# Performance work log

Measured on AMD Instinct MI355X. Metric: run time of the kernel, lower is better.

Reference implementation:

```python
import jax, jax.numpy as jnp
import numpy as np

ROI = 31            # roi_size (odd)
HALF = ROI // 2     # tf.cast(roi_size/2, int32) == 15


def setup_inputs() -> dict:
    key = jax.random.key(0)
    k1, k2, k3, k4 = jax.random.split(key, 4)
    B, H, W, C, N = 16, 256, 256, 32, 4096
    encoded_poses = jax.random.normal(k1, (B, H, W, C), dtype=jnp.float32)
    b = jax.random.randint(k2, (N, 1), 0, B)
    y = jax.random.randint(k3, (N, 1), 0, H)
    x = jax.random.randint(k4, (N, 1), 0, W)
    roi_centers = jnp.concatenate([b, y, x], axis=1).astype(jnp.int32)
    return {"encoded_poses": encoded_poses, "roi_centers": roi_centers}


def reference(encoded_poses, roi_centers):
    # encoded_poses: [B, H, W, C]; roi_centers: [N, 3] = (batch, y, x)
    H, W = encoded_poses.shape[1], encoded_poses.shape[2]
    off = jnp.arange(ROI, dtype=roi_centers.dtype) - HALF          # [ROI]
    b = roi_centers[:, 0]                                          # [N]
    rows = roi_centers[:, 1, None] + off                           # [N, ROI]
    cols = roi_centers[:, 2, None] + off                           # [N, ROI]
    # Out-of-bounds positions get zero padding (as in tf.pad of the original).
    rmask = (rows >= 0) & (rows < H)
    cmask = (cols >= 0) & (cols < W)
    rc = jnp.clip(rows, 0, H - 1)
    cc = jnp.clip(cols, 0, W - 1)
    # Batched gather: [N, ROI, ROI, C]
    cuts = encoded_poses[b[:, None, None], rc[:, :, None], cc[:, None, :], :]
    mask = (rmask[:, :, None] & cmask[:, None, :])[..., None]
    return jnp.where(mask, cuts, jnp.zeros((), dtype=cuts.dtype))
```

## Files before the change

kernel.cpp:

```cpp
#include <hip/hip_runtime.h>

#define ROI 31
#define HALF 15
#define H_DIM 256
#define W_DIM 256
#define C_DIM 32
#define NBKT 4096

typedef float vfloat4 __attribute__((ext_vector_type(4)));

__global__ __launch_bounds__(1024) void sort_kernel(
    const int* __restrict__ centers, int* __restrict__ perm,
    int* __restrict__ off, int N)
{
    __shared__ int hist[NBKT];
    __shared__ int base[NBKT];
    __shared__ int partial[1024];
    const int t = threadIdx.x;

    for (int k = t; k < NBKT; k += 1024) hist[k] = 0;
    __syncthreads();

    for (int i = t; i < N; i += 1024) {
        const int key = (centers[3 * i] << 8) | centers[3 * i + 1];
        atomicAdd(&hist[key], 1);
    }
    __syncthreads();

    const int s0 = hist[4 * t], s1 = hist[4 * t + 1];
    const int s2 = hist[4 * t + 2], s3 = hist[4 * t + 3];
    const int loc = s0 + s1 + s2 + s3;
    partial[t] = loc;
    __syncthreads();
    for (int o = 1; o < 1024; o <<= 1) {
        int v = (t >= o) ? partial[t - o] : 0;
        __syncthreads();
        partial[t] += v;
        __syncthreads();
    }
    const int ex = partial[t] - loc;
    base[4 * t]     = ex;
    base[4 * t + 1] = ex + s0;
    base[4 * t + 2] = ex + s0 + s1;
    base[4 * t + 3] = ex + s0 + s1 + s2;
    __syncthreads();

    for (int k = t; k < NBKT; k += 1024) off[k] = base[k];
    if (t == 0) off[NBKT] = N;
    for (int k = t; k < NBKT; k += 1024) hist[k] = 0;
    __syncthreads();

    for (int i = t; i < N; i += 1024) {
        const int key = (centers[3 * i] << 8) | centers[3 * i + 1];
        const int pos = base[key] + atomicAdd(&hist[key], 1);
        perm[pos] = i;
    }
}

__global__ __launch_bounds__(256) void strip_scatter_kernel(
    const float* __restrict__ poses, const int* __restrict__ centers,
    const int* __restrict__ perm, const int* __restrict__ off,
    float* __restrict__ out)
{
    __shared__ vfloat4 row_lds[W_DIM * C_DIM / 4];

    const int strip = blockIdx.x;
    const int b  = strip >> 8;
    const int rr = strip & (H_DIM - 1);
    const int t  = threadIdx.x;

    const vfloat4* src_row = reinterpret_cast<const vfloat4*>(
        poses + ((size_t)b * H_DIM + rr) * W_DIM * C_DIM);
    #pragma unroll
    for (int i = 0; i < 8; ++i)
        row_lds[i * 256 + t] = src_row[i * 256 + t];
    __syncthreads();

    const int ylo = max(rr - HALF, 0), yhi = min(rr + HALF, H_DIM - 1);
    const int start = off[(b << 8) | ylo];
    const int end   = off[((b << 8) | yhi) + 1];

    const int pc = t >> 3;
    const int q  = t & 7;
    if (pc >= ROI) return;

    for (int pos = start; pos < end; ++pos) {
        const int n = perm[pos];
        const int y = centers[3 * n + 1];
        const int x = centers[3 * n + 2];
        const int r  = rr - (y - HALF);
        const int cc = x - HALF + pc;
        const bool cok = (cc >= 0) && (cc < W_DIM);
        const int ccc = min(max(cc, 0), W_DIM - 1);
        vfloat4 v = cok ? row_lds[ccc * 8 + q] : (vfloat4)0.0f;
        float* dst = out + (((size_t)n * ROI + r) * ROI + pc) * C_DIM + q * 4;
        __builtin_nontemporal_store(v, reinterpret_cast<vfloat4*>(dst));
    }
}

__global__ __launch_bounds__(256) void zero_rows_kernel(
    const int* __restrict__ centers, float* __restrict__ out)
{
    const int n = blockIdx.x;
    const int y = centers[3 * n + 1];
    if (y >= HALF && y <= H_DIM - 1 + HALF - ROI + 1) {  }
    const int t = threadIdx.x;
    if (t >= ROI * (C_DIM / 4)) return;
    const int pc = t >> 3;
    const int q  = t & 7;
    const vfloat4 z = (vfloat4)0.0f;

    const int rlo_end   = max(HALF - y, 0);
    const int rhi_start = min(H_DIM - 1 + HALF - y + 1, ROI);
    for (int r = 0; r < rlo_end; ++r) {
        float* dst = out + (((size_t)n * ROI + r) * ROI + pc) * C_DIM + q * 4;
        __builtin_nontemporal_store(z, reinterpret_cast<vfloat4*>(dst));
    }
    for (int r = rhi_start; r < ROI; ++r) {
        float* dst = out + (((size_t)n * ROI + r) * ROI + pc) * C_DIM + q * 4;
        __builtin_nontemporal_store(z, reinterpret_cast<vfloat4*>(dst));
    }
}

extern "C" void kernel_launch(void* const* d_in, const int* in_sizes, int n_in,
                              void* d_out, int out_size, void* d_ws, size_t ws_size,
                              hipStream_t stream) {
    const float* poses   = (const float*)d_in[0];
    const int*   centers = (const int*)d_in[1];
    float*       out     = (float*)d_out;

    const int N = in_sizes[1] / 3;
    const int B = in_sizes[0] / (H_DIM * W_DIM * C_DIM);

    int* perm = (int*)d_ws;
    int* off  = perm + N;

    sort_kernel<<<dim3(1), dim3(1024), 0, stream>>>(centers, perm, off, N);
    strip_scatter_kernel<<<dim3(B * H_DIM), dim3(256), 0, stream>>>(poses, centers, perm, off, out);
    zero_rows_kernel<<<dim3(N), dim3(256), 0, stream>>>(centers, out);
}
```

Measured before the change: 116.4 us.

## Fuse border zero-fill into strip scatter and pack center coords into sort records

The strip grid gains virtual rows above and below the image, so the same scatter kernel writes zeros for out-of-range ROI rows. This removes the separate zero_rows kernel and its launch. The sort also emits packed (index, y, x) records, so the scatter loop no longer does a dependent gather from perm into centers. In exchange, 30 extra strip blocks per batch do store-only work, and the packing limits N to what fits above 16 bits.

```diff
diff --git a/kernel.cpp b/kernel.cpp
--- a/kernel.cpp
+++ b/kernel.cpp
@@ -6,11 +6,12 @@
 #define W_DIM 256
 #define C_DIM 32
 #define NBKT 4096
+#define VROWS (H_DIM + 2*HALF)
 
 typedef float vfloat4 __attribute__((ext_vector_type(4)));
 
 __global__ __launch_bounds__(1024) void sort_kernel(
-    const int* __restrict__ centers, int* __restrict__ perm,
+    const int* __restrict__ centers, int* __restrict__ sorted,
     int* __restrict__ off, int N)
 {
     __shared__ int hist[NBKT];
@@ -51,30 +52,33 @@
     __syncthreads();
 
     for (int i = t; i < N; i += 1024) {
-        const int key = (centers[3 * i] << 8) | centers[3 * i + 1];
+        const int b = centers[3 * i], y = centers[3 * i + 1], x = centers[3 * i + 2];
+        const int key = (b << 8) | y;
         const int pos = base[key] + atomicAdd(&hist[key], 1);
-        perm[pos] = i;
+        sorted[pos] = (i << 16) | (y << 8) | x;
     }
 }
 
 __global__ __launch_bounds__(256) void strip_scatter_kernel(
-    const float* __restrict__ poses, const int* __restrict__ centers,
-    const int* __restrict__ perm, const int* __restrict__ off,
-    float* __restrict__ out)
+    const float* __restrict__ poses, const int* __restrict__ sorted,
+    const int* __restrict__ off, float* __restrict__ out)
 {
     __shared__ vfloat4 row_lds[W_DIM * C_DIM / 4];
 
     const int strip = blockIdx.x;
-    const int b  = strip >> 8;
-    const int rr = strip & (H_DIM - 1);
+    const int b  = strip / VROWS;
+    const int rr = strip % VROWS - HALF;
     const int t  = threadIdx.x;
+    const bool real = ((unsigned)rr < (unsigned)H_DIM);
 
-    const vfloat4* src_row = reinterpret_cast<const vfloat4*>(
-        poses + ((size_t)b * H_DIM + rr) * W_DIM * C_DIM);
-    #pragma unroll
-    for (int i = 0; i < 8; ++i)
-        row_lds[i * 256 + t] = src_row[i * 256 + t];
-    __syncthreads();
+    if (real) {
+        const vfloat4* src_row = reinterpret_cast<const vfloat4*>(
+            poses + ((size_t)b * H_DIM + rr) * W_DIM * C_DIM);
+        #pragma unroll
+        for (int i = 0; i < 8; ++i)
+            row_lds[i * 256 + t] = src_row[i * 256 + t];
+        __syncthreads();
+    }
 
     const int ylo = max(rr - HALF, 0), yhi = min(rr + HALF, H_DIM - 1);
     const int start = off[(b << 8) | ylo];
@@ -85,40 +89,20 @@
     if (pc >= ROI) return;
 
     for (int pos = start; pos < end; ++pos) {
-        const int n = perm[pos];
-        const int y = centers[3 * n + 1];
-        const int x = centers[3 * n + 2];
+        const int rec = sorted[pos];
+        const int n = rec >> 16;
+        const int y = (rec >> 8) & 255;
+        const int x = rec & 255;
         const int r  = rr - (y - HALF);
         const int cc = x - HALF + pc;
-        const bool cok = (cc >= 0) && (cc < W_DIM);
-        const int ccc = min(max(cc, 0), W_DIM - 1);
-        vfloat4 v = cok ? row_lds[ccc * 8 + q] : (vfloat4)0.0f;
+        vfloat4 v = (vfloat4)0.0f;
+        if (real) {
+            const bool cok = (cc >= 0) && (cc < W_DIM);
+            const int ccc = min(max(cc, 0), W_DIM - 1);
+            if (cok) v = row_lds[ccc * 8 + q];
+        }
         float* dst = out + (((size_t)n * ROI + r) * ROI + pc) * C_DIM + q * 4;
         __builtin_nontemporal_store(v, reinterpret_cast<vfloat4*>(dst));
-    }
-}
-
-__global__ __launch_bounds__(256) void zero_rows_kernel(
-    const int* __restrict__ centers, float* __restrict__ out)
-{
-    const int n = blockIdx.x;
-    const int y = centers[3 * n + 1];
-    if (y >= HALF && y <= H_DIM - 1 + HALF - ROI + 1) {  }
-    const int t = threadIdx.x;
-    if (t >= ROI * (C_DIM / 4)) return;
-    const int pc = t >> 3;
-    const int q  = t & 7;
-    const vfloat4 z = (vfloat4)0.0f;
-
-    const int rlo_end   = max(HALF - y, 0);
-    const int rhi_start = min(H_DIM - 1 + HALF - y + 1, ROI);
-    for (int r = 0; r < rlo_end; ++r) {
-        float* dst = out + (((size_t)n * ROI + r) * ROI + pc) * C_DIM + q * 4;
-        __builtin_nontemporal_store(z, reinterpret_cast<vfloat4*>(dst));
-    }
-    for (int r = rhi_start; r < ROI; ++r) {
-        float* dst = out + (((size_t)n * ROI + r) * ROI + pc) * C_DIM + q * 4;
-        __builtin_nontemporal_store(z, reinterpret_cast<vfloat4*>(dst));
     }
 }
 
@@ -132,10 +116,9 @@
     const int N = in_sizes[1] / 3;
     const int B = in_sizes[0] / (H_DIM * W_DIM * C_DIM);
 
-    int* perm = (int*)d_ws;
-    int* off  = perm + N;
+    int* sorted = (int*)d_ws;
+    int* off    = sorted + N;
 
-    sort_kernel<<<dim3(1), dim3(1024), 0, stream>>>(centers, perm, off, N);
-    strip_scatter_kernel<<<dim3(B * H_DIM), dim3(256), 0, stream>>>(poses, centers, perm, off, out);
-    zero_rows_kernel<<<dim3(N), dim3(256), 0, stream>>>(centers, out);
+    sort_kernel<<<dim3(1), dim3(1024), 0, stream>>>(centers, sorted, off, N);
+    strip_scatter_kernel<<<dim3(B * VROWS), dim3(256), 0, stream>>>(poses, sorted, off, out);
 }
```

New measurement: 113.5 us. 2.5% less time.
